# Kernel optimization log

Hardware: AMD Instinct MI355X
Metric: run time of the kernel (lower is better)

The kernel has to match this reference:

```python
import jax, jax.numpy as jnp
import numpy as np

H, HKV, D = 16, 4, 64
ROPE_BASE = 10000.0
EPS = 1e-6


def _rms_norm(x):
    return x * jax.lax.rsqrt(jnp.mean(x * x, axis=-1, keepdims=True) + EPS)


def _rope_cos_sin(T, dtype):
    inv_freq = 1.0 / (ROPE_BASE ** (jnp.arange(0, D, 2, dtype=jnp.float32) / D))  # [D/2]
    t = jnp.arange(T, dtype=jnp.float32)
    freqs = jnp.outer(t, inv_freq)  # [T, D/2]
    return jnp.cos(freqs)[None, :, None, :].astype(dtype), jnp.sin(freqs)[None, :, None, :].astype(dtype)


def _apply_rope(x, cos, sin):
    d = x.shape[-1] // 2
    x1, x2 = x[..., :d], x[..., d:]
    return jnp.concatenate([x1 * cos + x2 * sin, -x1 * sin + x2 * cos], axis=-1)


def setup_inputs() -> dict:
    key = jax.random.key(0)
    ks = jax.random.split(key, 6)
    B, T, dm = 1, 2048, 1024
    x = jax.random.normal(ks[0], (B, T, dm), dtype=jnp.float32)
    q_w = jax.random.normal(ks[1], (H * D, dm), dtype=jnp.float32) * 0.02
    k_w = jax.random.normal(ks[2], (HKV * D, dm), dtype=jnp.float32) * 0.02
    v_w = jax.random.normal(ks[3], (HKV * D, dm), dtype=jnp.float32) * 0.02
    o_w = jax.random.normal(ks[4], (dm, H * D), dtype=jnp.float32) * 0.02
    temp = jnp.ones((H,), dtype=jnp.float32) * np.sqrt(D)  # per-head temperature buffer
    curvature = jnp.asarray(1.0, dtype=jnp.float32)
    return {"x": x, "q_w": q_w, "k_w": k_w, "v_w": v_w, "o_w": o_w, "temp": temp, "curvature": curvature}


def reference(x, q_w, k_w, v_w, o_w, temp, curvature):
    B, T, dm = x.shape
    # projections
    q = (x @ q_w.T).reshape(B, T, H, D)
    k = (x @ k_w.T).reshape(B, T, HKV, D)
    v = (x @ v_w.T).reshape(B, T, HKV, D)
    q, k = _rms_norm(q), _rms_norm(k)
    cos, sin = _rope_cos_sin(T, q.dtype)
    q = _apply_rope(q, cos, sin)
    k = _apply_rope(k, cos, sin)
    # GQA: repeat kv heads
    rep = H // HKV
    k = jnp.repeat(k, rep, axis=2)  # [B,T,H,D]
    v = jnp.repeat(v, rep, axis=2)
    c = curvature
    # hyperboloid lift: time component x0 = sqrt(1/c + ||x||^2)
    q0 = jnp.sqrt(1.0 / c + jnp.sum(q * q, axis=-1))  # [B,T,H]
    k0 = jnp.sqrt(1.0 / c + jnp.sum(k * k, axis=-1))
    # Minkowski inner product <q,k>_L = q.k_spatial - q0*k0  -> [B,H,Tq,Tk]
    mink = jnp.einsum('bqhd,bkhd->bhqk', q, k) - q0.transpose(0, 2, 1)[..., :, None] * k0.transpose(0, 2, 1)[..., None, :]
    # Lorentz distance d = arccosh(clamp(-c*<q,k>_L, 1+eps)) / sqrt(c)
    dist = jnp.arccosh(jnp.maximum(-c * mink, 1.0 + 1e-5)) / jnp.sqrt(c)
    scores = -dist / temp[None, :, None, None]
    causal = jnp.tril(jnp.ones((T, T), dtype=bool))
    scores = jnp.where(causal[None, None], scores, -jnp.inf)
    w = jax.nn.softmax(scores, axis=-1)  # [B,H,Tq,Tk]
    attn = jnp.einsum('bhqk,bkhd->bqhd', w, v).reshape(B, T, H * D)
    out = attn @ o_w.T  # [B,T,dm]
    spatial_norm = jnp.mean(jnp.sqrt(jnp.sum(q * q, axis=-1)))
    return out, spatial_norm
```

## Files before the change

kernel.cpp:

```cpp
#include <hip/hip_runtime.h>
#include <hip/hip_bf16.h>

typedef __attribute__((ext_vector_type(8))) short short8;
typedef __attribute__((ext_vector_type(4))) short bf16x4;
typedef __attribute__((ext_vector_type(4))) float f32x4;

#define TT 2048
#define DM 1024
#define NH 16
#define NKV 4
#define HD 64

#define MFMA32(a,b,c) __builtin_amdgcn_mfma_f32_16x16x32_bf16(a,b,c,0,0,0)
#define MFMA16(a,b,c) __builtin_amdgcn_mfma_f32_16x16x16bf16_1k(a,b,c,0,0,0)

__device__ __forceinline__ unsigned short f2bf(float x){
  unsigned int u = __float_as_uint(x);
  u += 0x7fffu + ((u >> 16) & 1u);
  return (unsigned short)(u >> 16);
}
__device__ __forceinline__ unsigned int pkbf2(float x, float y){
  union { __hip_bfloat162 h; unsigned int u; } t;
  t.h = __float22bfloat162_rn(make_float2(x, y));
  return t.u;
}
__device__ __forceinline__ void gl_lds16(const unsigned short* g, unsigned short* l){
  __builtin_amdgcn_global_load_lds(
      (__attribute__((address_space(1))) void*)g,
      (__attribute__((address_space(3))) void*)l, 16, 0, 0);
}

__global__ __launch_bounds__(256) void convertw_kernel(
    const float* __restrict__ x,
    const float* __restrict__ qw, const float* __restrict__ kw,
    const float* __restrict__ vw, const float* __restrict__ ow,
    unsigned short* __restrict__ xb,
    unsigned short* __restrict__ wqkv, unsigned short* __restrict__ owb){
  long v = (long)blockIdx.x * 256 + threadIdx.x;
  const float* src; unsigned short* dst; long base;
  if      (v < 524288) { src = x;  dst = xb;             base = v; }
  else if (v < 786432) { src = qw; dst = wqkv;           base = v - 524288; }
  else if (v < 851968) { src = kw; dst = wqkv + 1048576; base = v - 786432; }
  else if (v < 917504) { src = vw; dst = wqkv + 1310720; base = v - 851968; }
  else                 { src = ow; dst = owb;            base = v - 917504; }
  f32x4 d = *(const f32x4*)(src + base * 4);
  uint2 pk = { pkbf2(d[0], d[1]), pkbf2(d[2], d[3]) };
  *(uint2*)(dst + base * 4) = pk;
}

__global__ __launch_bounds__(256) void gemm1_fused(
    const unsigned short* __restrict__ xb, const unsigned short* __restrict__ wqkv,
    unsigned short* __restrict__ qb, unsigned short* __restrict__ kb,
    unsigned short* __restrict__ vt,
    float* __restrict__ q0, float* __restrict__ k0,
    float* __restrict__ bpart, const float* __restrict__ curv){
  __shared__ __align__(16) unsigned short AB[2 * 8192];
  __shared__ float bsum;
  unsigned short* As = AB;
  unsigned short* Bs = AB + 8192;
  float* Ct = (float*)AB;
  const int tid = threadIdx.x, lane = tid & 63, wave = tid >> 6;
  const int hIdx = blockIdx.x;
  const int bm = blockIdx.y * 64, bn = hIdx * 64;
  const int wm = (wave >> 1) * 32, wn = (wave & 1) * 32;
  const int ml = lane & 15, quad = lane >> 4;
  if (tid == 0) bsum = 0.f;
  f32x4 acc[2][2];
  const f32x4 z = {0.f, 0.f, 0.f, 0.f};
  acc[0][0] = z; acc[0][1] = z; acc[1][0] = z; acc[1][1] = z;

  const int srow = wave * 16 + (lane >> 2), scol = (lane & 3) * 8;
  const unsigned short* Ag = xb   + (long)(bm + srow) * 1024 + scol;
  const unsigned short* Bg = wqkv + (long)(bn + srow) * 1024 + scol;

#define G1_STAGE(nb, ko)                                           \
  do {                                                             \
    gl_lds16(Ag + (ko),      As + (nb) * 4096 + wave * 512);       \
    gl_lds16(Ag + (ko) + 32, As + (nb) * 4096 + 2048 + wave * 512);\
    gl_lds16(Bg + (ko),      Bs + (nb) * 4096 + wave * 512);       \
    gl_lds16(Bg + (ko) + 32, Bs + (nb) * 4096 + 2048 + wave * 512);\
  } while (0)

#define G1_COMPUTE(b)                                                   \
  do {                                                                  \
    _Pragma("unroll")                                                   \
    for (int half = 0; half < 2; half++){                               \
      const unsigned short* Ah = As + (b) * 4096 + half * 2048;         \
      const unsigned short* Bh = Bs + (b) * 4096 + half * 2048;         \
      short8 a0f = *(const short8*)&Ah[(wm + ml) * 32 + quad * 8];      \
      short8 a1f = *(const short8*)&Ah[(wm + 16 + ml) * 32 + quad * 8]; \
      short8 b0f = *(const short8*)&Bh[(wn + ml) * 32 + quad * 8];      \
      short8 b1f = *(const short8*)&Bh[(wn + 16 + ml) * 32 + quad * 8]; \
      acc[0][0] = MFMA32(a0f, b0f, acc[0][0]);                          \
      acc[0][1] = MFMA32(a0f, b1f, acc[0][1]);                          \
      acc[1][0] = MFMA32(a1f, b0f, acc[1][0]);                          \
      acc[1][1] = MFMA32(a1f, b1f, acc[1][1]);                          \
    }                                                                   \
  } while (0)

  G1_STAGE(0, 0);
  __syncthreads();
  for (int kk = 0; kk < 1024; kk += 128){
    G1_STAGE(1, kk + 64);
    G1_COMPUTE(0);
    __syncthreads();
    if (kk + 128 < 1024) G1_STAGE(0, kk + 128);
    G1_COMPUTE(1);
    __syncthreads();
  }
#undef G1_STAGE
#undef G1_COMPUTE

#pragma unroll
  for (int i = 0; i < 2; i++)
#pragma unroll
    for (int j = 0; j < 2; j++)
#pragma unroll
      for (int r = 0; r < 4; r++)
        Ct[(wm + i * 16 + quad * 4 + r) * 65 + wn + j * 16 + ml] = acc[i][j][r];
  __syncthreads();

  if (hIdx < 20){
    const bool isq = hIdx < 16;
    const int h = isq ? hIdx : hIdx - 16;
    const float c = curv[0];
    unsigned short* ob = isq ? qb : kb;
    float* o0 = isq ? q0 : k0;
#pragma unroll 1
    for (int rr = 0; rr < 16; rr++){
      const int row = wave * 16 + rr;
      const int t = bm + row;
      float val = Ct[row * 65 + lane];
      float ss = val * val;
#pragma unroll
      for (int off = 1; off < 64; off <<= 1) ss += __shfl_xor(ss, off);
      float scale = __builtin_amdgcn_rsqf(ss * (1.f / 64.f) + 1e-6f);
      float xn = val * scale;
      float other = __shfl_xor(xn, 32);
      int fi = lane & 31;
      float ang = (float)t * __builtin_amdgcn_exp2f((float)fi * (-13.287712379549449f / 32.f));
      float sn, cs; __sincosf(ang, &sn, &cs);
      float outv = (lane < 32) ? (xn * cs + other * sn) : (xn * cs - other * sn);
      ob[((long)h * TT + t) * 64 + lane] = f2bf(outv);
      if (lane == 0){
        float sq = ss * scale * scale;
        o0[h * TT + t] = __builtin_amdgcn_sqrtf(1.f / c + sq);
        if (isq) atomicAdd(&bsum, __builtin_amdgcn_sqrtf(sq));
      }
    }
  } else {
    const int hk = hIdx - 20;
    const int d = tid >> 2, tseg = (tid & 3) * 16;
    uint4 w0, w1;
    w0.x = pkbf2(Ct[(tseg + 0) * 65 + d], Ct[(tseg + 1) * 65 + d]);
    w0.y = pkbf2(Ct[(tseg + 2) * 65 + d], Ct[(tseg + 3) * 65 + d]);
    w0.z = pkbf2(Ct[(tseg + 4) * 65 + d], Ct[(tseg + 5) * 65 + d]);
    w0.w = pkbf2(Ct[(tseg + 6) * 65 + d], Ct[(tseg + 7) * 65 + d]);
    w1.x = pkbf2(Ct[(tseg + 8) * 65 + d], Ct[(tseg + 9) * 65 + d]);
    w1.y = pkbf2(Ct[(tseg +10) * 65 + d], Ct[(tseg +11) * 65 + d]);
    w1.z = pkbf2(Ct[(tseg +12) * 65 + d], Ct[(tseg +13) * 65 + d]);
    w1.w = pkbf2(Ct[(tseg +14) * 65 + d], Ct[(tseg +15) * 65 + d]);
    const int tile = (bm + tseg) >> 4;
    unsigned short* dst = vt + ((long)(hk * 128 + tile) * 64 + d) * 16;
    *(uint4*)dst = w0;
    *(uint4*)(dst + 8) = w1;
  }
  __syncthreads();
  if (tid == 0) bpart[blockIdx.y * 24 + hIdx] = bsum;
}

__global__ __launch_bounds__(256, 3) void attn_kernel(
    const unsigned short* __restrict__ qb_, const unsigned short* __restrict__ kb_,
    const unsigned short* __restrict__ vt_,
    const float* __restrict__ q0_, const float* __restrict__ k0_,
    const float* __restrict__ temp, const float* __restrict__ curv,
    unsigned short* __restrict__ attn_out,
    const float* __restrict__ bpart, float* __restrict__ out_scalar){
  __shared__ float lds[8 * 1104];
  const int tid = threadIdx.x, lane = tid & 63, wave = tid >> 6;
  const int qt  = 127 - (blockIdx.x >> 3);
  const int sub = blockIdx.x & 7;
  const int kvh = sub >> 1, hp = sub & 1;
  const int h0 = kvh * 4 + hp * 2, h1 = h0 + 1;
  const int i0 = qt * 16;
  const int ml = lane & 15, quad = lane >> 4;
  const float c = curv[0];
  const float rsc = __builtin_amdgcn_rsqf(c);
  const float fac0 = -rsc / temp[h0];
  const float fac1 = -rsc / temp[h1];
  const f32x4 z = {0.f, 0.f, 0.f, 0.f};
  const unsigned short* kh = kb_ + (long)kvh * TT * 64;
  const unsigned short* vh = vt_ + (long)kvh * 128 * 1024;
  const float* k0h = k0_ + kvh * TT;

  short8 qa0 = *(const short8*)&qb_[((long)h0 * TT + i0 + ml) * 64 + quad * 8];
  short8 qa1 = *(const short8*)&qb_[((long)h0 * TT + i0 + ml) * 64 + 32 + quad * 8];
  short8 qb0 = *(const short8*)&qb_[((long)h1 * TT + i0 + ml) * 64 + quad * 8];
  short8 qb1 = *(const short8*)&qb_[((long)h1 * TT + i0 + ml) * 64 + 32 + quad * 8];
  const float q0c0 = c * q0_[h0 * TT + i0 + ml];
  const float q0c1 = c * q0_[h1 * TT + i0 + ml];
  const int rowq = i0 + ml;

  f32x4 o0[4], o1[4];
#pragma unroll
  for (int dt = 0; dt < 4; dt++){ o0[dt] = z; o1[dt] = z; }
  float l0 = 0.f, l1 = 0.f;

  const int nt = (i0 + 47) >> 5;

#pragma unroll 1
  for (int t = wave; t < nt; t += 4){
    const int j0 = t << 5;
    const unsigned short* kp = kh + (long)j0 * 64;
    short8 ka0 = *(const short8*)(kp + ml * 64 + quad * 8);
    short8 ka1 = *(const short8*)(kp + ml * 64 + 32 + quad * 8);
    short8 kc0 = *(const short8*)(kp + (16 + ml) * 64 + quad * 8);
    short8 kc1 = *(const short8*)(kp + (16 + ml) * 64 + 32 + quad * 8);
    f32x4 k0a = *(const f32x4*)(k0h + j0 + quad * 4);
    f32x4 k0b = *(const f32x4*)(k0h + j0 + 16 + quad * 4);
    const unsigned short* vpa = vh + (long)(j0 >> 4) * 1024;
    bf16x4 vfa0 = *(const bf16x4*)(vpa + ( 0 + ml) * 16 + quad * 4);
    bf16x4 vfa1 = *(const bf16x4*)(vpa + (16 + ml) * 16 + quad * 4);
    bf16x4 vfa2 = *(const bf16x4*)(vpa + (32 + ml) * 16 + quad * 4);
    bf16x4 vfa3 = *(const bf16x4*)(vpa + (48 + ml) * 16 + quad * 4);
    bf16x4 vfb0 = *(const bf16x4*)(vpa + 1024 + ( 0 + ml) * 16 + quad * 4);
    bf16x4 vfb1 = *(const bf16x4*)(vpa + 1024 + (16 + ml) * 16 + quad * 4);
    bf16x4 vfb2 = *(const bf16x4*)(vpa + 1024 + (32 + ml) * 16 + quad * 4);
    bf16x4 vfb3 = *(const bf16x4*)(vpa + 1024 + (48 + ml) * 16 + quad * 4);

    const int keyb = j0 + quad * 4;
    const bool nm = (j0 + 31 > i0);
    {
      f32x4 s0 = z, s1 = z;
      s0 = MFMA32(ka0, qa0, s0);
      s0 = MFMA32(ka1, qa1, s0);
      s1 = MFMA32(kc0, qa0, s1);
      s1 = MFMA32(kc1, qa1, s1);
      float p0[4], p1[4];
#pragma unroll
      for (int r = 0; r < 4; r++){
        float argA = fmaxf(__builtin_fmaf(-c, s0[r], q0c0 * k0a[r]), 1.00001f);
        float wA   = argA + __builtin_amdgcn_sqrtf(__builtin_fmaf(argA, argA, -1.f));
        float pA   = __builtin_amdgcn_exp2f(fac0 * __builtin_amdgcn_logf(wA));
        float argB = fmaxf(__builtin_fmaf(-c, s1[r], q0c0 * k0b[r]), 1.00001f);
        float wB   = argB + __builtin_amdgcn_sqrtf(__builtin_fmaf(argB, argB, -1.f));
        float pB   = __builtin_amdgcn_exp2f(fac0 * __builtin_amdgcn_logf(wB));
        if (nm){
          if (keyb + r > rowq)      pA = 0.f;
          if (keyb + 16 + r > rowq) pB = 0.f;
        }
        p0[r] = pA; p1[r] = pB;
        l0 += pA + pB;
      }
      uint2 pua = { pkbf2(p0[0], p0[1]), pkbf2(p0[2], p0[3]) };
      uint2 pub = { pkbf2(p1[0], p1[1]), pkbf2(p1[2], p1[3]) };
      bf16x4 pfa = *(bf16x4*)&pua;
      bf16x4 pfb = *(bf16x4*)&pub;
      o0[0] = MFMA16(vfa0, pfa, o0[0]);
      o0[1] = MFMA16(vfa1, pfa, o0[1]);
      o0[2] = MFMA16(vfa2, pfa, o0[2]);
      o0[3] = MFMA16(vfa3, pfa, o0[3]);
      o0[0] = MFMA16(vfb0, pfb, o0[0]);
      o0[1] = MFMA16(vfb1, pfb, o0[1]);
      o0[2] = MFMA16(vfb2, pfb, o0[2]);
      o0[3] = MFMA16(vfb3, pfb, o0[3]);
    }
    {
      f32x4 s0 = z, s1 = z;
      s0 = MFMA32(ka0, qb0, s0);
      s0 = MFMA32(ka1, qb1, s0);
      s1 = MFMA32(kc0, qb0, s1);
      s1 = MFMA32(kc1, qb1, s1);
      float p0[4], p1[4];
#pragma unroll
      for (int r = 0; r < 4; r++){
        float argA = fmaxf(__builtin_fmaf(-c, s0[r], q0c1 * k0a[r]), 1.00001f);
        float wA   = argA + __builtin_amdgcn_sqrtf(__builtin_fmaf(argA, argA, -1.f));
        float pA   = __builtin_amdgcn_exp2f(fac1 * __builtin_amdgcn_logf(wA));
        float argB = fmaxf(__builtin_fmaf(-c, s1[r], q0c1 * k0b[r]), 1.00001f);
        float wB   = argB + __builtin_amdgcn_sqrtf(__builtin_fmaf(argB, argB, -1.f));
        float pB   = __builtin_amdgcn_exp2f(fac1 * __builtin_amdgcn_logf(wB));
        if (nm){
          if (keyb + r > rowq)      pA = 0.f;
          if (keyb + 16 + r > rowq) pB = 0.f;
        }
        p0[r] = pA; p1[r] = pB;
        l1 += pA + pB;
      }
      uint2 pua = { pkbf2(p0[0], p0[1]), pkbf2(p0[2], p0[3]) };
      uint2 pub = { pkbf2(p1[0], p1[1]), pkbf2(p1[2], p1[3]) };
      bf16x4 pfa = *(bf16x4*)&pua;
      bf16x4 pfb = *(bf16x4*)&pub;
      o1[0] = MFMA16(vfa0, pfa, o1[0]);
      o1[1] = MFMA16(vfa1, pfa, o1[1]);
      o1[2] = MFMA16(vfa2, pfa, o1[2]);
      o1[3] = MFMA16(vfa3, pfa, o1[3]);
      o1[0] = MFMA16(vfb0, pfb, o1[0]);
      o1[1] = MFMA16(vfb1, pfb, o1[1]);
      o1[2] = MFMA16(vfb2, pfb, o1[2]);
      o1[3] = MFMA16(vfb3, pfb, o1[3]);
    }
  }
  l0 += __shfl_xor(l0, 16); l0 += __shfl_xor(l0, 32);
  l1 += __shfl_xor(l1, 16); l1 += __shfl_xor(l1, 32);
  {
    float* w0 = lds + wave * 1104;
    float* w1 = lds + (4 + wave) * 1104;
#pragma unroll
    for (int dt = 0; dt < 4; dt++){
      *(f32x4*)&w0[ml * 68 + dt * 16 + quad * 4] = o0[dt];
      *(f32x4*)&w1[ml * 68 + dt * 16 + quad * 4] = o1[dt];
    }
    if (quad == 0){ w0[1088 + ml] = l0; w1[1088 + ml] = l1; }
  }
  __syncthreads();
  {
    const int row = tid >> 4, c0 = (tid & 15) * 4;
#pragma unroll 1
    for (int hb = 0; hb < 2; hb++){
      const float* base = lds + hb * 4 * 1104;
      float L = 0.f; f32x4 s = z;
#pragma unroll
      for (int w = 0; w < 4; w++){
        const float* rg = base + w * 1104;
        L += rg[1088 + row];
        f32x4 t2 = *(const f32x4*)&rg[row * 68 + c0];
        s[0] += t2[0]; s[1] += t2[1]; s[2] += t2[2]; s[3] += t2[3];
      }
      float invL = __builtin_amdgcn_rcpf(L);
      const int h = hb ? h1 : h0;
      uint2 o = { pkbf2(s[0] * invL, s[1] * invL), pkbf2(s[2] * invL, s[3] * invL) };
      *(uint2*)&attn_out[(long)(i0 + row) * 1024 + h * 64 + c0] = o;
    }
  }
  if (blockIdx.x == 0 && tid < 64){
    float s = 0.f;
    for (int i = lane; i < 768; i += 64) s += bpart[i];
#pragma unroll
    for (int off = 1; off < 64; off <<= 1) s += __shfl_xor(s, off);
    if (lane == 0) out_scalar[0] = s * (1.f / 32768.f);
  }
}

__global__ __launch_bounds__(256) void gemm2_kernel(
    const unsigned short* __restrict__ A, const unsigned short* __restrict__ B,
    float* __restrict__ C){
  __shared__ __align__(16) unsigned short As[2 * 4096];
  __shared__ __align__(16) unsigned short Bs[2 * 4096];
  const int tid = threadIdx.x, lane = tid & 63, wave = tid >> 6;
  const int bm = blockIdx.y * 64, bn = blockIdx.x * 64;
  const int wm = (wave >> 1) * 32, wn = (wave & 1) * 32;
  const int ml = lane & 15, quad = lane >> 4;
  f32x4 acc[2][2];
  const f32x4 z = {0.f, 0.f, 0.f, 0.f};
  acc[0][0] = z; acc[0][1] = z; acc[1][0] = z; acc[1][1] = z;

  const int srow = wave * 16 + (lane >> 2), scol = (lane & 3) * 8;
  const unsigned short* Ag = A + (long)(bm + srow) * 1024 + scol;
  const unsigned short* Bg = B + (long)(bn + srow) * 1024 + scol;

#define G2_STAGE(nb, ko)                                           \
  do {                                                             \
    gl_lds16(Ag + (ko),      As + (nb) * 4096 + wave * 512);       \
    gl_lds16(Ag + (ko) + 32, As + (nb) * 4096 + 2048 + wave * 512);\
    gl_lds16(Bg + (ko),      Bs + (nb) * 4096 + wave * 512);       \
    gl_lds16(Bg + (ko) + 32, Bs + (nb) * 4096 + 2048 + wave * 512);\
  } while (0)

#define G2_COMPUTE(b)                                                   \
  do {                                                                  \
    _Pragma("unroll")                                                   \
    for (int half = 0; half < 2; half++){                               \
      const unsigned short* Ah = As + (b) * 4096 + half * 2048;         \
      const unsigned short* Bh = Bs + (b) * 4096 + half * 2048;         \
      short8 a0f = *(const short8*)&Ah[(wm + ml) * 32 + quad * 8];      \
      short8 a1f = *(const short8*)&Ah[(wm + 16 + ml) * 32 + quad * 8]; \
      short8 b0f = *(const short8*)&Bh[(wn + ml) * 32 + quad * 8];      \
      short8 b1f = *(const short8*)&Bh[(wn + 16 + ml) * 32 + quad * 8]; \
      acc[0][0] = MFMA32(a0f, b0f, acc[0][0]);                          \
      acc[0][1] = MFMA32(a0f, b1f, acc[0][1]);                          \
      acc[1][0] = MFMA32(a1f, b0f, acc[1][0]);                          \
      acc[1][1] = MFMA32(a1f, b1f, acc[1][1]);                          \
    }                                                                   \
  } while (0)

  G2_STAGE(0, 0);
  __syncthreads();
  for (int kk = 0; kk < 1024; kk += 128){
    G2_STAGE(1, kk + 64);
    G2_COMPUTE(0);
    __syncthreads();
    if (kk + 128 < 1024) G2_STAGE(0, kk + 128);
    G2_COMPUTE(1);
    __syncthreads();
  }
#undef G2_STAGE
#undef G2_COMPUTE

#pragma unroll
  for (int i = 0; i < 2; i++)
#pragma unroll
    for (int j = 0; j < 2; j++)
#pragma unroll
      for (int r = 0; r < 4; r++)
        C[(long)(bm + wm + i * 16 + quad * 4 + r) * 1024 + bn + wn + j * 16 + ml] = acc[i][j][r];
}

extern "C" void kernel_launch(void* const* d_in, const int* in_sizes, int n_in,
                              void* d_out, int out_size, void* d_ws, size_t ws_size,
                              hipStream_t stream){
  const float* x    = (const float*)d_in[0];
  const float* qw   = (const float*)d_in[1];
  const float* kw   = (const float*)d_in[2];
  const float* vw   = (const float*)d_in[3];
  const float* ow   = (const float*)d_in[4];
  const float* temp = (const float*)d_in[5];
  const float* curv = (const float*)d_in[6];
  float* out = (float*)d_out;

  char* ws = (char*)d_ws;
  size_t off = 0;
  auto alloc = [&](size_t bytes) -> char* {
    char* p = ws + off;
    off += (bytes + 255) & ~(size_t)255;
    return p;
  };
  unsigned short* xb   = (unsigned short*)alloc((size_t)TT * DM * 2);
  unsigned short* wqkv = (unsigned short*)alloc((size_t)1536 * DM * 2);
  unsigned short* owb  = (unsigned short*)alloc((size_t)DM * DM * 2);
  unsigned short* qb   = (unsigned short*)alloc((size_t)NH * TT * HD * 2);
  unsigned short* kb   = (unsigned short*)alloc((size_t)NKV * TT * HD * 2);
  unsigned short* vt   = (unsigned short*)alloc((size_t)NKV * TT * HD * 2);
  float*          q0   = (float*)alloc((size_t)NH * TT * 4);
  float*          k0   = (float*)alloc((size_t)NKV * TT * 4);
  unsigned short* attn = (unsigned short*)alloc((size_t)TT * DM * 2);
  float*          bpart= (float*)alloc((size_t)768 * 4);

  convertw_kernel<<<4608, 256, 0, stream>>>(x, qw, kw, vw, ow, xb, wqkv, owb);
  gemm1_fused<<<dim3(24, 32), 256, 0, stream>>>(xb, wqkv, qb, kb, vt, q0, k0, bpart, curv);
  attn_kernel<<<1024, 256, 0, stream>>>(qb, kb, vt, q0, k0, temp, curv, attn,
                                        bpart, out + (size_t)TT * DM);
  gemm2_kernel<<<dim3(16, 32), 256, 0, stream>>>(attn, owb, out);
}
```

Before: 147.6 us.

## Enlarge gemm1 tile to 128x64 and run epilogue directly from registers

The QKV projection kernel now uses 128-row tiles, with each wave owning 32 full-width rows, and grid rows are halved. The RMS-norm, RoPE and V-transpose epilogue now works on the MFMA accumulators in registers with 16-lane shuffles, so the LDS staging of C and its extra barrier are gone. The main loop drops the double buffering and uses a single buffer with two barriers per 64-wide k step, which may expose load latency. The bpart reduction count is updated to match the smaller grid.

```diff
diff --git a/kernel.cpp b/kernel.cpp
--- a/kernel.cpp
+++ b/kernel.cpp
@@ -54,116 +54,106 @@
     unsigned short* __restrict__ vt,
     float* __restrict__ q0, float* __restrict__ k0,
     float* __restrict__ bpart, const float* __restrict__ curv){
-  __shared__ __align__(16) unsigned short AB[2 * 8192];
+  __shared__ __align__(16) unsigned short As[2 * 128 * 32];
+  __shared__ __align__(16) unsigned short Bs[2 * 64 * 32];
   __shared__ float bsum;
-  unsigned short* As = AB;
-  unsigned short* Bs = AB + 8192;
-  float* Ct = (float*)AB;
   const int tid = threadIdx.x, lane = tid & 63, wave = tid >> 6;
   const int hIdx = blockIdx.x;
-  const int bm = blockIdx.y * 64, bn = hIdx * 64;
-  const int wm = (wave >> 1) * 32, wn = (wave & 1) * 32;
+  const int bm = blockIdx.y * 128, bn = hIdx * 64;
   const int ml = lane & 15, quad = lane >> 4;
   if (tid == 0) bsum = 0.f;
-  f32x4 acc[2][2];
+  f32x4 acc[2][4];
   const f32x4 z = {0.f, 0.f, 0.f, 0.f};
-  acc[0][0] = z; acc[0][1] = z; acc[1][0] = z; acc[1][1] = z;
-
-  const int srow = wave * 16 + (lane >> 2), scol = (lane & 3) * 8;
-  const unsigned short* Ag = xb   + (long)(bm + srow) * 1024 + scol;
-  const unsigned short* Bg = wqkv + (long)(bn + srow) * 1024 + scol;
-
-#define G1_STAGE(nb, ko)                                           \
-  do {                                                             \
-    gl_lds16(Ag + (ko),      As + (nb) * 4096 + wave * 512);       \
-    gl_lds16(Ag + (ko) + 32, As + (nb) * 4096 + 2048 + wave * 512);\
-    gl_lds16(Bg + (ko),      Bs + (nb) * 4096 + wave * 512);       \
-    gl_lds16(Bg + (ko) + 32, Bs + (nb) * 4096 + 2048 + wave * 512);\
-  } while (0)
-
-#define G1_COMPUTE(b)                                                   \
-  do {                                                                  \
-    _Pragma("unroll")                                                   \
-    for (int half = 0; half < 2; half++){                               \
-      const unsigned short* Ah = As + (b) * 4096 + half * 2048;         \
-      const unsigned short* Bh = Bs + (b) * 4096 + half * 2048;         \
-      short8 a0f = *(const short8*)&Ah[(wm + ml) * 32 + quad * 8];      \
-      short8 a1f = *(const short8*)&Ah[(wm + 16 + ml) * 32 + quad * 8]; \
-      short8 b0f = *(const short8*)&Bh[(wn + ml) * 32 + quad * 8];      \
-      short8 b1f = *(const short8*)&Bh[(wn + 16 + ml) * 32 + quad * 8]; \
-      acc[0][0] = MFMA32(a0f, b0f, acc[0][0]);                          \
-      acc[0][1] = MFMA32(a0f, b1f, acc[0][1]);                          \
-      acc[1][0] = MFMA32(a1f, b0f, acc[1][0]);                          \
-      acc[1][1] = MFMA32(a1f, b1f, acc[1][1]);                          \
-    }                                                                   \
-  } while (0)
-
-  G1_STAGE(0, 0);
-  __syncthreads();
-  for (int kk = 0; kk < 1024; kk += 128){
-    G1_STAGE(1, kk + 64);
-    G1_COMPUTE(0);
+#pragma unroll
+  for (int i = 0; i < 2; i++)
+#pragma unroll
+    for (int j = 0; j < 4; j++) acc[i][j] = z;
+
+  const int srow = tid >> 2, scol = (tid & 3) * 8;
+  const unsigned short* Ag0 = xb   + (long)(bm + srow) * 1024 + scol;
+  const unsigned short* Ag1 = Ag0 + 64 * 1024;
+  const unsigned short* Bg  = wqkv + (long)(bn + srow) * 1024 + scol;
+  unsigned short* Asw = As + wave * 512;
+  unsigned short* Bsw = Bs + wave * 512;
+
+  for (int kk = 0; kk < 1024; kk += 64){
     __syncthreads();
-    if (kk + 128 < 1024) G1_STAGE(0, kk + 128);
-    G1_COMPUTE(1);
+    gl_lds16(Ag0 + kk,      Asw);
+    gl_lds16(Ag1 + kk,      Asw + 2048);
+    gl_lds16(Bg  + kk,      Bsw);
+    gl_lds16(Ag0 + kk + 32, Asw + 4096);
+    gl_lds16(Ag1 + kk + 32, Asw + 4096 + 2048);
+    gl_lds16(Bg  + kk + 32, Bs + 2048 + wave * 512);
     __syncthreads();
-  }
-#undef G1_STAGE
-#undef G1_COMPUTE
-
-#pragma unroll
-  for (int i = 0; i < 2; i++)
-#pragma unroll
-    for (int j = 0; j < 2; j++)
-#pragma unroll
-      for (int r = 0; r < 4; r++)
-        Ct[(wm + i * 16 + quad * 4 + r) * 65 + wn + j * 16 + ml] = acc[i][j][r];
-  __syncthreads();
+#pragma unroll
+    for (int half = 0; half < 2; half++){
+      const unsigned short* Ah = As + half * 4096;
+      const unsigned short* Bh = Bs + half * 2048;
+      short8 a0 = *(const short8*)&Ah[(wave * 32 + ml) * 32 + quad * 8];
+      short8 a1 = *(const short8*)&Ah[(wave * 32 + 16 + ml) * 32 + quad * 8];
+      short8 b0 = *(const short8*)&Bh[(ml) * 32 + quad * 8];
+      short8 b1 = *(const short8*)&Bh[(16 + ml) * 32 + quad * 8];
+      short8 b2 = *(const short8*)&Bh[(32 + ml) * 32 + quad * 8];
+      short8 b3 = *(const short8*)&Bh[(48 + ml) * 32 + quad * 8];
+      acc[0][0] = MFMA32(a0, b0, acc[0][0]);
+      acc[0][1] = MFMA32(a0, b1, acc[0][1]);
+      acc[0][2] = MFMA32(a0, b2, acc[0][2]);
+      acc[0][3] = MFMA32(a0, b3, acc[0][3]);
+      acc[1][0] = MFMA32(a1, b0, acc[1][0]);
+      acc[1][1] = MFMA32(a1, b1, acc[1][1]);
+      acc[1][2] = MFMA32(a1, b2, acc[1][2]);
+      acc[1][3] = MFMA32(a1, b3, acc[1][3]);
+    }
+  }
 
   if (hIdx < 20){
     const bool isq = hIdx < 16;
     const int h = isq ? hIdx : hIdx - 16;
     const float c = curv[0];
     unsigned short* ob = isq ? qb : kb;
-    float* o0 = isq ? q0 : k0;
-#pragma unroll 1
-    for (int rr = 0; rr < 16; rr++){
-      const int row = wave * 16 + rr;
-      const int t = bm + row;
-      float val = Ct[row * 65 + lane];
-      float ss = val * val;
-#pragma unroll
-      for (int off = 1; off < 64; off <<= 1) ss += __shfl_xor(ss, off);
-      float scale = __builtin_amdgcn_rsqf(ss * (1.f / 64.f) + 1e-6f);
-      float xn = val * scale;
-      float other = __shfl_xor(xn, 32);
-      int fi = lane & 31;
-      float ang = (float)t * __builtin_amdgcn_exp2f((float)fi * (-13.287712379549449f / 32.f));
-      float sn, cs; __sincosf(ang, &sn, &cs);
-      float outv = (lane < 32) ? (xn * cs + other * sn) : (xn * cs - other * sn);
-      ob[((long)h * TT + t) * 64 + lane] = f2bf(outv);
-      if (lane == 0){
-        float sq = ss * scale * scale;
-        o0[h * TT + t] = __builtin_amdgcn_sqrtf(1.f / c + sq);
-        if (isq) atomicAdd(&bsum, __builtin_amdgcn_sqrtf(sq));
+    float* o0p = isq ? q0 : k0;
+    const float if0 = __builtin_amdgcn_exp2f((float)ml        * (-13.287712379549449f / 32.f));
+    const float if1 = __builtin_amdgcn_exp2f((float)(16 + ml) * (-13.287712379549449f / 32.f));
+    float bl = 0.f;
+#pragma unroll
+    for (int i = 0; i < 2; i++){
+#pragma unroll
+      for (int r = 0; r < 4; r++){
+        const int t = bm + wave * 32 + i * 16 + quad * 4 + r;
+        float v0 = acc[i][0][r], v1 = acc[i][1][r], v2 = acc[i][2][r], v3 = acc[i][3][r];
+        float ss = v0 * v0 + v1 * v1 + v2 * v2 + v3 * v3;
+        ss += __shfl_xor(ss, 1); ss += __shfl_xor(ss, 2);
+        ss += __shfl_xor(ss, 4); ss += __shfl_xor(ss, 8);
+        float scale = __builtin_amdgcn_rsqf(ss * (1.f / 64.f) + 1e-6f);
+        float x0 = v0 * scale, x1 = v1 * scale, x2 = v2 * scale, x3 = v3 * scale;
+        float sn0, cs0, sn1, cs1;
+        __sincosf((float)t * if0, &sn0, &cs0);
+        __sincosf((float)t * if1, &sn1, &cs1);
+        unsigned short* op = ob + ((long)h * TT + t) * 64;
+        op[ml]      = f2bf( x0 * cs0 + x2 * sn0);
+        op[16 + ml] = f2bf( x1 * cs1 + x3 * sn1);
+        op[32 + ml] = f2bf( x2 * cs0 - x0 * sn0);
+        op[48 + ml] = f2bf( x3 * cs1 - x1 * sn1);
+        if (ml == 0){
+          float sq = ss * scale * scale;
+          o0p[h * TT + t] = __builtin_amdgcn_sqrtf(1.f / c + sq);
+          if (isq) bl += __builtin_amdgcn_sqrtf(sq);
+        }
       }
     }
+    if (isq && ml == 0) atomicAdd(&bsum, bl);
   } else {
     const int hk = hIdx - 20;
-    const int d = tid >> 2, tseg = (tid & 3) * 16;
-    uint4 w0, w1;
-    w0.x = pkbf2(Ct[(tseg + 0) * 65 + d], Ct[(tseg + 1) * 65 + d]);
-    w0.y = pkbf2(Ct[(tseg + 2) * 65 + d], Ct[(tseg + 3) * 65 + d]);
-    w0.z = pkbf2(Ct[(tseg + 4) * 65 + d], Ct[(tseg + 5) * 65 + d]);
-    w0.w = pkbf2(Ct[(tseg + 6) * 65 + d], Ct[(tseg + 7) * 65 + d]);
-    w1.x = pkbf2(Ct[(tseg + 8) * 65 + d], Ct[(tseg + 9) * 65 + d]);
-    w1.y = pkbf2(Ct[(tseg +10) * 65 + d], Ct[(tseg +11) * 65 + d]);
-    w1.z = pkbf2(Ct[(tseg +12) * 65 + d], Ct[(tseg +13) * 65 + d]);
-    w1.w = pkbf2(Ct[(tseg +14) * 65 + d], Ct[(tseg +15) * 65 + d]);
-    const int tile = (bm + tseg) >> 4;
-    unsigned short* dst = vt + ((long)(hk * 128 + tile) * 64 + d) * 16;
-    *(uint4*)dst = w0;
-    *(uint4*)(dst + 8) = w1;
+#pragma unroll
+    for (int i = 0; i < 2; i++){
+      const int tile = (bm >> 4) + wave * 2 + i;
+#pragma unroll
+      for (int j = 0; j < 4; j++){
+        uint2 w2 = { pkbf2(acc[i][j][0], acc[i][j][1]), pkbf2(acc[i][j][2], acc[i][j][3]) };
+        unsigned short* dst = vt + ((long)(hk * 128 + tile) * 64 + j * 16 + ml) * 16 + quad * 4;
+        *(uint2*)dst = w2;
+      }
+    }
   }
   __syncthreads();
   if (tid == 0) bpart[blockIdx.y * 24 + hIdx] = bsum;
@@ -335,7 +325,7 @@
   }
   if (blockIdx.x == 0 && tid < 64){
     float s = 0.f;
-    for (int i = lane; i < 768; i += 64) s += bpart[i];
+    for (int i = lane; i < 384; i += 64) s += bpart[i];
 #pragma unroll
     for (int off = 1; off < 64; off <<= 1) s += __shfl_xor(s, off);
     if (lane == 0) out_scalar[0] = s * (1.f / 32768.f);
@@ -437,7 +427,7 @@
   float*          bpart= (float*)alloc((size_t)768 * 4);
 
   convertw_kernel<<<4608, 256, 0, stream>>>(x, qw, kw, vw, ow, xb, wqkv, owb);
-  gemm1_fused<<<dim3(24, 32), 256, 0, stream>>>(xb, wqkv, qb, kb, vt, q0, k0, bpart, curv);
+  gemm1_fused<<<dim3(24, 16), 256, 0, stream>>>(xb, wqkv, qb, kb, vt, q0, k0, bpart, curv);
   attn_kernel<<<1024, 256, 0, stream>>>(qb, kb, vt, q0, k0, temp, curv, attn,
                                         bpart, out + (size_t)TT * DM);
   gemm2_kernel<<<dim3(16, 32), 256, 0, stream>>>(attn, owb, out);
```

Result: faster. 143.4 us (-2.8%).
